# Performance work log

Hardware: AMD Instinct MI355X
Metric: run time of the kernel (lower is better)

## Reference

```python
import jax, jax.numpy as jnp
import numpy as np

GROUP_SIZE = 128  # per-group quantization granularity along K


def setup_inputs() -> dict:
    key = jax.random.key(0)
    k1, k2, k3, k4 = jax.random.split(key, 4)
    B, S, K, N = 4, 2048, 4096, 11008
    num_groups = K // GROUP_SIZE
    x = jax.random.normal(k1, (B, S, K), dtype=jnp.float16)
    # packed uint4 pairs stored as bytes (values 0..255); int32 stands in for uint8
    weight = jax.random.randint(k2, (N, K // 2), 0, 256, dtype=jnp.int32)
    scale = jax.random.uniform(k3, (N, num_groups), dtype=jnp.float16, minval=0.001, maxval=0.02)
    bias = jax.random.normal(k4, (N,), dtype=jnp.float16)
    return {"x": x, "weight": weight, "scale": scale, "bias": bias}


def _dequant_int4(weight, scale):
    # weight: [N, K//2] packed bytes; low nibble = even k, high nibble = odd k
    N, Kh = weight.shape
    K = Kh * 2
    low = (weight & 15) - 8          # [N, K//2], signed int4 in [-8, 7]
    high = ((weight >> 4) & 15) - 8  # [N, K//2]
    w_int4 = jnp.stack([low, high], axis=-1).reshape(N, K).astype(jnp.float32)
    # broadcast per-group scales along K: [N, num_groups] -> [N, K]
    s = jnp.repeat(scale.astype(jnp.float32), GROUP_SIZE, axis=1)
    return w_int4 * s  # [N, K] fp32


def reference(x, weight, scale, bias):
    # out = x @ dequant(w).T + bias, fp32 accumulation, fp16 store (as in kernel)
    w_fp = _dequant_int4(weight, scale)                     # [N, K]
    acc = jnp.einsum('bsk,nk->bsn', x.astype(jnp.float32), w_fp)
    acc = acc + bias.astype(jnp.float32)[None, None, :]
    return acc.astype(jnp.float16)
```

## Files before the change

kernel.cpp:

```cpp
#include <hip/hip_runtime.h>

#define DEVINL __device__ __forceinline__

typedef __bf16 bf16x8 __attribute__((ext_vector_type(8)));
typedef float  f32x4  __attribute__((ext_vector_type(4)));

constexpr int KK = 4096;
constexpr int NN = 11008;
constexpr int NG = 32;

DEVINL unsigned short f2bf(float f){
  union { float f; unsigned u; } v; v.f = f;
  unsigned r = v.u + 0x7FFF + ((v.u >> 16) & 1);
  return (unsigned short)(r >> 16);
}
DEVINL unsigned pack2(float lo, float hi){
  return (unsigned)f2bf(lo) | ((unsigned)f2bf(hi) << 16);
}
DEVINL void gload16(const void* g, void* l){
  __builtin_amdgcn_global_load_lds(
      (const __attribute__((address_space(1))) void*)g,
      (__attribute__((address_space(3))) void*)l, 16, 0, 0);
}

__global__ __launch_bounds__(256) void k_dequant(const int* __restrict__ W,
                                                 const float* __restrict__ S,
                                                 unsigned short* __restrict__ WB){
  int t = blockIdx.x * 256 + threadIdx.x;
  int row = t >> 9;
  int kp0 = (t & 511) << 2;
  int g   = kp0 >> 6;
  float s = S[row * NG + g];
  const int4 p = reinterpret_cast<const int4*>(W)[t];
  const int* pb = reinterpret_cast<const int*>(&p);
  unsigned q[4];
  #pragma unroll
  for (int i = 0; i < 4; ++i){
    int b = pb[i];
    float lo = ((float)(b & 15)        - 8.0f) * s;
    float hi = ((float)((b >> 4) & 15) - 8.0f) * s;
    q[i] = pack2(lo, hi);
  }
  reinterpret_cast<int4*>(WB)[t] = make_int4((int)q[0], (int)q[1], (int)q[2], (int)q[3]);
}

__global__ __launch_bounds__(256) void k_cvtA(const float* __restrict__ X,
                                              unsigned short* __restrict__ XB){
  int t = blockIdx.x * 256 + threadIdx.x;
  const float4* src = reinterpret_cast<const float4*>(X) + (size_t)t * 2;
  float4 a = src[0], b = src[1];
  reinterpret_cast<int4*>(XB)[t] = make_int4(
      (int)pack2(a.x, a.y), (int)pack2(a.z, a.w),
      (int)pack2(b.x, b.y), (int)pack2(b.z, b.w));
}

constexpr int BM2 = 256, BN2 = 256, BK2 = 32;
constexpr int PBY = 16384;
constexpr int BUFBY = 32768;

#define VW(N)  asm volatile("s_waitcnt vmcnt(" #N ")" ::: "memory")
#define BAR()  do { __builtin_amdgcn_s_barrier(); asm volatile("" ::: "memory"); } while (0)

__global__ __launch_bounds__(1024, 1) void k_gemm16b(const unsigned short* __restrict__ A,
                                                     const unsigned short* __restrict__ B,
                                                     const float* __restrict__ Bias,
                                                     float* __restrict__ C){
  __shared__ char smem[131072];
  const int tid = threadIdx.x, lane = tid & 63, wid = tid >> 6;
  const int wm = wid >> 2, wn = wid & 3;
  const int lr = lane & 15, hi = lane >> 4;
  const int cpx = gridDim.x >> 3;
  const int wg  = (blockIdx.x & 7) * cpx + (blockIdx.x >> 3);
  const int NTT = NN / BN2;
  const int mt = wg / NTT, nt = wg % NTT;
  const char* Ab = (const char*)(A + (size_t)mt * BM2 * KK);
  const char* Bb = (const char*)(B + (size_t)nt * BN2 * KK);
  const int srow  = tid >> 2;
  const int scolb = (tid & 2) ? ((tid & 1) ? 48 : 32) : ((tid & 1) ? 16 : 0);

  auto stage = [&](int buf, int kt){
    const int sw = ((srow >> 1) & 3) << 4;
    const char* srcA = Ab + (size_t)srow * (KK * 2) + kt * (BK2 * 2) + (scolb ^ sw);
    gload16(srcA, smem + buf * BUFBY + tid * 16);
    const char* srcB = Bb + (size_t)srow * (KK * 2) + kt * (BK2 * 2) + (scolb ^ sw);
    gload16(srcB, smem + buf * BUFBY + PBY + tid * 16);
  };
  auto frag = [&](int buf, int isB, int row) -> bf16x8 {
    return *reinterpret_cast<const bf16x8*>(
        smem + buf * BUFBY + isB * PBY + row * 64
             + ((hi * 16) ^ (((row >> 1) & 3) << 4)));
  };

  f32x4 acc[4][4] = {};

  const int NT = KK / BK2;
  stage(0, 0); stage(1, 1); stage(2, 2);
  VW(4);
  BAR();

  auto tile_body = [&](int t){
    const int buf = t & 3;
    if (t + 3 < NT) stage((t + 3) & 3, t + 3);
    bf16x8 af[4], bf[4];
    #pragma unroll
    for (int i = 0; i < 4; ++i)
      af[i] = frag(buf, 0, wm*64 + i*16 + lr);
    #pragma unroll
    for (int j = 0; j < 4; ++j)
      bf[j] = frag(buf, 1, wn*64 + j*16 + lr);
    __builtin_amdgcn_s_setprio(1);
    #pragma unroll
    for (int i = 0; i < 4; ++i)
      #pragma unroll
      for (int j = 0; j < 4; ++j)
        acc[i][j] = __builtin_amdgcn_mfma_f32_16x16x32_bf16(af[i], bf[j], acc[i][j], 0, 0, 0);
    __builtin_amdgcn_s_setprio(0);
  };

  for (int t = 0; t < NT - 3; ++t){
    tile_body(t);
    VW(4);
    BAR();
  }
  tile_body(NT - 3); VW(2); BAR();
  tile_body(NT - 2); VW(0); BAR();
  tile_body(NT - 1);

  const int cmb = mt * BM2, cnb = nt * BN2;
  #pragma unroll
  for (int j = 0; j < 4; ++j){
    int col = cnb + wn * 64 + j * 16 + lr;
    float bv = Bias[col];
    #pragma unroll
    for (int i = 0; i < 4; ++i){
      int row0 = cmb + wm * 64 + i * 16 + hi * 4;
      #pragma unroll
      for (int r = 0; r < 4; ++r)
        C[(size_t)(row0 + r) * NN + col] = acc[i][j][r] + bv;
    }
  }
}

constexpr int BM = 128, BN = 128, BK = 32;
__global__ __launch_bounds__(256) void k_gemm_ws(const float* __restrict__ A,
                                                 const unsigned short* __restrict__ B,
                                                 const float* __restrict__ Bias,
                                                 float* __restrict__ C){
  __shared__ unsigned short As[2][BM][BK];
  __shared__ unsigned short Bs[2][BN][BK];
  const int tid = threadIdx.x;
  const int NT = NN / BN;
  const int mt = blockIdx.x / NT, nt = blockIdx.x % NT;
  const float*          Ab = A + (size_t)mt * BM * KK;
  const unsigned short* Bb = B + (size_t)nt * BN * KK;
  const int lane = tid & 63, wid = tid >> 6;
  const int wm = wid >> 1, wn = wid & 1;
  const int lr = lane & 15, lk = (lane >> 4) << 3;

  auto ld = [&](int kt, float4* ra, int4* rb){
    #pragma unroll
    for (int r = 0; r < 2; ++r){
      int c = r * 256 + tid, row = c >> 2, k0 = (c & 3) << 3;
      const float* src = Ab + (size_t)row * KK + kt * BK + k0;
      ra[2*r]   = *reinterpret_cast<const float4*>(src);
      ra[2*r+1] = *reinterpret_cast<const float4*>(src + 4);
      rb[r] = *reinterpret_cast<const int4*>(Bb + (size_t)row * KK + kt * BK + k0);
    }
  };
  auto st = [&](int buf, const float4* ra, const int4* rb){
    #pragma unroll
    for (int r = 0; r < 2; ++r){
      int c = r * 256 + tid, row = c >> 2, k0 = (c & 3) << 3;
      unsigned q[4];
      #pragma unroll
      for (int i = 0; i < 4; ++i)
        q[i] = pack2(ra[2*r + (i >> 1)][(i & 1) * 2], ra[2*r + (i >> 1)][(i & 1) * 2 + 1]);
      *reinterpret_cast<int4*>(&As[buf][row][k0]) =
          make_int4((int)q[0], (int)q[1], (int)q[2], (int)q[3]);
      *reinterpret_cast<int4*>(&Bs[buf][row][k0]) = rb[r];
    }
  };

  f32x4 acc[4][4] = {};
  {
    float4 ra[4]; int4 rb[2];
    ld(0, ra, rb);
    st(0, ra, rb);
  }
  __syncthreads();
  const int KT = KK / BK;
  for (int kt = 0; kt < KT; ++kt){
    int cur = kt & 1;
    float4 na[4]; int4 nb[2];
    if (kt + 1 < KT) ld(kt + 1, na, nb);
    bf16x8 af[4], bfr[4];
    #pragma unroll
    for (int i = 0; i < 4; ++i)
      af[i] = *reinterpret_cast<const bf16x8*>(&As[cur][wm*64 + i*16 + lr][lk]);
    #pragma unroll
    for (int i = 0; i < 4; ++i)
      bfr[i] = *reinterpret_cast<const bf16x8*>(&Bs[cur][wn*64 + i*16 + lr][lk]);
    #pragma unroll
    for (int i = 0; i < 4; ++i)
      #pragma unroll
      for (int j = 0; j < 4; ++j)
        acc[i][j] = __builtin_amdgcn_mfma_f32_16x16x32_bf16(af[i], bfr[j], acc[i][j], 0, 0, 0);
    if (kt + 1 < KT) st(cur ^ 1, na, nb);
    __syncthreads();
  }
  const int cm = mt * BM + wm * 64;
  const int cn = nt * BN + wn * 64;
  float bv[4];
  #pragma unroll
  for (int j = 0; j < 4; ++j) bv[j] = Bias[cn + j*16 + lr];
  #pragma unroll
  for (int i = 0; i < 4; ++i)
    #pragma unroll
    for (int j = 0; j < 4; ++j)
      #pragma unroll
      for (int r = 0; r < 4; ++r){
        size_t rr = (size_t)(cm + i*16 + (lane >> 4)*4 + r);
        C[rr * NN + (cn + j*16 + lr)] = acc[i][j][r] + bv[j];
      }
}

extern "C" void kernel_launch(void* const* d_in, const int* in_sizes, int n_in,
                              void* d_out, int out_size, void* d_ws, size_t ws_size,
                              hipStream_t stream){
  const float* x    = (const float*)d_in[0];
  const int*   w    = (const int*)d_in[1];
  const float* s    = (const float*)d_in[2];
  const float* bias = (const float*)d_in[3];
  float* out = (float*)d_out;
  const int M = in_sizes[0] / KK;
  const size_t needW = (size_t)NN * KK * 2;
  const size_t needA = (size_t)M * KK * 2;
  const int dq_blocks = (NN * (KK / 8)) / 256;

  if (ws_size >= needW + needA && (M % BM2) == 0){
    unsigned short* wb = (unsigned short*)d_ws;
    unsigned short* xb = (unsigned short*)((char*)d_ws + needW);
    k_dequant<<<dq_blocks, 256, 0, stream>>>(w, s, wb);
    k_cvtA<<<(M * (KK / 8)) / 256, 256, 0, stream>>>(x, xb);
    const int grid16 = (M / BM2) * (NN / BN2);
    k_gemm16b<<<grid16, 1024, 0, stream>>>(xb, wb, bias, out);
  } else {
    unsigned short* wb = (unsigned short*)d_ws;
    k_dequant<<<dq_blocks, 256, 0, stream>>>(w, s, wb);
    const int grid = (M / BM) * (NN / BN);
    k_gemm_ws<<<grid, 256, 0, stream>>>(x, wb, bias, out);
  }
}
```

Baseline: 767.5 us.

## Rework bf16 GEMM into 8-wave ping-pong with BK=64 split-stage prefetch

Measured after the change: 785.5 us. +2.4%, slower.

```diff
diff --git a/kernel.cpp b/kernel.cpp
--- a/kernel.cpp
+++ b/kernel.cpp
@@ -54,17 +54,17 @@
       (int)pack2(b.x, b.y), (int)pack2(b.z, b.w));
 }
 
-constexpr int BM2 = 256, BN2 = 256, BK2 = 32;
-constexpr int PBY = 16384;
-constexpr int BUFBY = 32768;
+constexpr int BM2 = 256, BN2 = 256, BK2 = 64;
+constexpr int SLOT = 16384;
+constexpr int BUFBY = 65536;
 
 #define VW(N)  asm volatile("s_waitcnt vmcnt(" #N ")" ::: "memory")
 #define BAR()  do { __builtin_amdgcn_s_barrier(); asm volatile("" ::: "memory"); } while (0)
 
-__global__ __launch_bounds__(1024, 1) void k_gemm16b(const unsigned short* __restrict__ A,
-                                                     const unsigned short* __restrict__ B,
-                                                     const float* __restrict__ Bias,
-                                                     float* __restrict__ C){
+__global__ __launch_bounds__(512, 1) void k_gemm_kp(const unsigned short* __restrict__ A,
+                                                    const unsigned short* __restrict__ B,
+                                                    const float* __restrict__ Bias,
+                                                    float* __restrict__ C){
   __shared__ char smem[131072];
   const int tid = threadIdx.x, lane = tid & 63, wid = tid >> 6;
   const int wm = wid >> 2, wn = wid & 3;
@@ -75,56 +75,81 @@
   const int mt = wg / NTT, nt = wg % NTT;
   const char* Ab = (const char*)(A + (size_t)mt * BM2 * KK);
   const char* Bb = (const char*)(B + (size_t)nt * BN2 * KK);
-  const int srow  = tid >> 2;
-  const int scolb = (tid & 2) ? ((tid & 1) ? 48 : 32) : ((tid & 1) ? 16 : 0);
-
-  auto stage = [&](int buf, int kt){
-    const int sw = ((srow >> 1) & 3) << 4;
-    const char* srcA = Ab + (size_t)srow * (KK * 2) + kt * (BK2 * 2) + (scolb ^ sw);
-    gload16(srcA, smem + buf * BUFBY + tid * 16);
-    const char* srcB = Bb + (size_t)srow * (KK * 2) + kt * (BK2 * 2) + (scolb ^ sw);
-    gload16(srcB, smem + buf * BUFBY + PBY + tid * 16);
-  };
-  auto frag = [&](int buf, int isB, int row) -> bf16x8 {
+
+  auto stage = [&](int buf, int slot, int isB, int kt, int h){
+    const char* base = isB ? Bb : Ab;
+    #pragma unroll
+    for (int r = 0; r < 2; ++r){
+      int row = r * 128 + (tid >> 2);
+      int scolb = (tid & 3) * 16;
+      const char* src = base + (size_t)row * (KK * 2) + (kt * 64 + h * 32) * 2
+                      + (scolb ^ (((row >> 1) & 3) << 4));
+      char* dst = smem + buf * BUFBY + slot * SLOT + r * 8192 + tid * 16;
+      gload16(src, dst);
+    }
+  };
+  auto frag = [&](int buf, int slot, int row) -> bf16x8 {
     return *reinterpret_cast<const bf16x8*>(
-        smem + buf * BUFBY + isB * PBY + row * 64
+        smem + buf * BUFBY + slot * SLOT + row * 64
              + ((hi * 16) ^ (((row >> 1) & 3) << 4)));
   };
 
-  f32x4 acc[4][4] = {};
-
-  const int NT = KK / BK2;
-  stage(0, 0); stage(1, 1); stage(2, 2);
+  bf16x8 af[4], bf[4];
+  f32x4 acc[8][4] = {};
+
+  auto rdA = [&](int buf, int slot, int i0){
+    #pragma unroll
+    for (int i = 0; i < 4; ++i)
+      af[i] = frag(buf, slot, wm*128 + (i0 + i)*16 + lr);
+  };
+  auto rdB = [&](int buf, int slot){
+    #pragma unroll
+    for (int j = 0; j < 4; ++j)
+      bf[j] = frag(buf, slot, wn*64 + j*16 + lr);
+  };
+  auto MM = [&](int i0){
+    __builtin_amdgcn_s_setprio(1);
+    #pragma unroll
+    for (int i = 0; i < 4; ++i)
+      #pragma unroll
+      for (int j = 0; j < 4; ++j)
+        acc[i0 + i][j] = __builtin_amdgcn_mfma_f32_16x16x32_bf16(af[i], bf[j], acc[i0 + i][j], 0, 0, 0);
+    __builtin_amdgcn_s_setprio(0);
+  };
+
+  stage(0, 0, 0, 0, 0); stage(0, 1, 1, 0, 0);
+  stage(0, 2, 0, 0, 1); stage(0, 3, 1, 0, 1);
+  stage(1, 0, 0, 1, 0); stage(1, 1, 1, 1, 0);
   VW(4);
   BAR();
 
-  auto tile_body = [&](int t){
-    const int buf = t & 3;
-    if (t + 3 < NT) stage((t + 3) & 3, t + 3);
-    bf16x8 af[4], bf[4];
-    #pragma unroll
-    for (int i = 0; i < 4; ++i)
-      af[i] = frag(buf, 0, wm*64 + i*16 + lr);
-    #pragma unroll
-    for (int j = 0; j < 4; ++j)
-      bf[j] = frag(buf, 1, wn*64 + j*16 + lr);
-    __builtin_amdgcn_s_setprio(1);
-    #pragma unroll
-    for (int i = 0; i < 4; ++i)
-      #pragma unroll
-      for (int j = 0; j < 4; ++j)
-        acc[i][j] = __builtin_amdgcn_mfma_f32_16x16x32_bf16(af[i], bf[j], acc[i][j], 0, 0, 0);
-    __builtin_amdgcn_s_setprio(0);
-  };
-
-  for (int t = 0; t < NT - 3; ++t){
-    tile_body(t);
-    VW(4);
-    BAR();
-  }
-  tile_body(NT - 3); VW(2); BAR();
-  tile_body(NT - 2); VW(0); BAR();
-  tile_body(NT - 1);
+  const int NT = KK / BK2;
+  for (int t = 0; t < NT; ++t){
+    const int buf = t & 1;
+    const bool p1f = (t + 1 < NT), p2f = (t + 2 < NT);
+    rdA(buf, 0, 0); rdB(buf, 1);
+    if (p1f) stage(buf ^ 1, 2, 0, t + 1, 1);
+    BAR();
+    MM(0);
+    BAR();
+    rdA(buf, 0, 4);
+    if (p1f) stage(buf ^ 1, 3, 1, t + 1, 1);
+    if (p1f) VW(4); else VW(0);
+    BAR();
+    MM(4);
+    BAR();
+    rdA(buf, 2, 0); rdB(buf, 3);
+    if (p2f) stage(buf, 0, 0, t + 2, 0);
+    BAR();
+    MM(0);
+    BAR();
+    rdA(buf, 2, 4);
+    if (p2f) stage(buf, 1, 1, t + 2, 0);
+    if (p2f) VW(4); else VW(0);
+    BAR();
+    MM(4);
+    BAR();
+  }
 
   const int cmb = mt * BM2, cnb = nt * BN2;
   #pragma unroll
@@ -132,8 +157,8 @@
     int col = cnb + wn * 64 + j * 16 + lr;
     float bv = Bias[col];
     #pragma unroll
-    for (int i = 0; i < 4; ++i){
-      int row0 = cmb + wm * 64 + i * 16 + hi * 4;
+    for (int i = 0; i < 8; ++i){
+      int row0 = cmb + wm * 128 + i * 16 + hi * 4;
       #pragma unroll
       for (int r = 0; r < 4; ++r)
         C[(size_t)(row0 + r) * NN + col] = acc[i][j][r] + bv;
@@ -242,8 +267,8 @@
     unsigned short* xb = (unsigned short*)((char*)d_ws + needW);
     k_dequant<<<dq_blocks, 256, 0, stream>>>(w, s, wb);
     k_cvtA<<<(M * (KK / 8)) / 256, 256, 0, stream>>>(x, xb);
-    const int grid16 = (M / BM2) * (NN / BN2);
-    k_gemm16b<<<grid16, 1024, 0, stream>>>(xb, wb, bias, out);
+    const int grid8 = (M / BM2) * (NN / BN2);
+    k_gemm_kp<<<grid8, 512, 0, stream>>>(xb, wb, bias, out);
   } else {
     unsigned short* wb = (unsigned short*)d_ws;
     k_dequant<<<dq_blocks, 256, 0, stream>>>(w, s, wb);
```
